# Kernel optimization log

Measured on AMD Instinct MI355X. Metric: run time of the kernel, lower is better.

The kernel has to match this reference:

```python
import jax, jax.numpy as jnp
import numpy as np

TIMESTEPS = 8
NUM_HEADS = 16
CTX = 1024
D = 1024
HD = D // NUM_HEADS
LN_EPS = 1e-5


def setup_inputs() -> dict:
    key = jax.random.key(0)
    ks = jax.random.split(key, 16)
    s = 0.02
    return {
        "current_embs": jax.random.normal(ks[0], (4, CTX, D), jnp.float32),
        "emb_table": jax.random.normal(ks[1], (TIMESTEPS, D), jnp.float32) * s,
        "Wq": jax.random.normal(ks[2], (NUM_HEADS, D, HD), jnp.float32) * s,
        "Wk": jax.random.normal(ks[3], (NUM_HEADS, D, HD), jnp.float32) * s,
        "Wv": jax.random.normal(ks[4], (NUM_HEADS, D, HD), jnp.float32) * s,
        "fc_w": jax.random.normal(ks[5], (D, D), jnp.float32) * s,
        "fc_b": jnp.zeros((D,), jnp.float32),
        "ln1_w": jnp.ones((D,), jnp.float32),
        "ln1_b": jnp.zeros((D,), jnp.float32),
        "ln2_w": jnp.ones((D,), jnp.float32),
        "ln2_b": jnp.zeros((D,), jnp.float32),
        "mlp_w1": jax.random.normal(ks[6], (D, 2 * D), jnp.float32) * s,
        "mlp_b1": jnp.zeros((2 * D,), jnp.float32),
        "mlp_w2": jax.random.normal(ks[7], (2 * D, D), jnp.float32) * s,
        "mlp_b2": jnp.zeros((D,), jnp.float32),
        "mlp_w3": jax.random.normal(ks[8], (D, D), jnp.float32) * s,
        "mlp_b3": jnp.zeros((D,), jnp.float32),
    }


def _layernorm(x, w, b):
    mu = jnp.mean(x, axis=-1, keepdims=True)
    var = jnp.var(x, axis=-1, keepdims=True)
    return (x - mu) * jax.lax.rsqrt(var + LN_EPS) * w + b


def _block(x, Wq, Wk, Wv, fc_w, fc_b, ln1_w, ln1_b, ln2_w, ln2_b,
           mlp_w1, mlp_b1, mlp_w2, mlp_b2, mlp_w3, mlp_b3):
    B, T, C = x.shape
    h = _layernorm(x, ln1_w, ln1_b)
    # per-head projections: [B,H,T,HD]
    q = jnp.einsum("btd,hdk->bhtk", h, Wq)
    k = jnp.einsum("btd,hdk->bhtk", h, Wk)
    v = jnp.einsum("btd,hdk->bhtk", h, Wv)
    # NOTE: original scales by embed_size**-0.5 (C), not head_dim**-0.5
    wei = jnp.einsum("bhtk,bhsk->bhts", q, k) * (C ** -0.5)
    causal = jnp.tril(jnp.ones((T, T), bool))
    wei = jnp.where(causal, wei, -jnp.inf)
    wei = jax.nn.softmax(wei, axis=-1)
    attn = jnp.einsum("bhts,bhsk->bhtk", wei, v)  # [B,H,T,HD]
    attn = attn.transpose(0, 2, 1, 3).reshape(B, T, C)  # concat heads
    sa = attn @ fc_w + fc_b
    x = x + sa  # dropout is identity in eval mode
    h2 = _layernorm(x, ln2_w, ln2_b)
    m = ((h2 @ mlp_w1 + mlp_b1) @ mlp_w2 + mlp_b2) @ mlp_w3 + mlp_b3
    m = jax.nn.gelu(m, approximate=False)  # GELU after three stacked Linears, as in source
    return x + m


def reference(current_embs, emb_table, Wq, Wk, Wv, fc_w, fc_b,
              ln1_w, ln1_b, ln2_w, ln2_b,
              mlp_w1, mlp_b1, mlp_w2, mlp_b2, mlp_w3, mlp_b3):
    new_embs = current_embs
    for i in range(TIMESTEPS):
        current_embs = current_embs + new_embs + emb_table[i][None, None, :]
        new_embs = _block(current_embs, Wq, Wk, Wv, fc_w, fc_b,
                          ln1_w, ln1_b, ln2_w, ln2_b,
                          mlp_w1, mlp_b1, mlp_w2, mlp_b2, mlp_w3, mlp_b3)
    return new_embs
```

## Files before the change

### kernel.cpp

```cpp
#include <hip/hip_runtime.h>
#include <hip/hip_bf16.h>
#include <math.h>

typedef __bf16 bf16;
typedef __bf16 bf16x8 __attribute__((ext_vector_type(8)));
typedef __bf16 bf16x4 __attribute__((ext_vector_type(4)));
typedef short  s16x4  __attribute__((ext_vector_type(4)));
typedef float  f32x4  __attribute__((ext_vector_type(4)));

#define MFMA32(a,b,c) __builtin_amdgcn_mfma_f32_16x16x32_bf16((a),(b),(c),0,0,0)
#define MFMA16(a,b,c) __builtin_amdgcn_mfma_f32_16x16x16bf16_1k((a),(b),(c),0,0,0)
#define EXP2F(x) __builtin_amdgcn_exp2f(x)
#define GLL16(gp, lp) __builtin_amdgcn_global_load_lds(\
    (const __attribute__((address_space(1))) void*)(gp), \
    (__attribute__((address_space(3))) void*)(lp), 16, 0, 0)

__device__ __forceinline__ float wave_sum(float v){
#pragma unroll
  for(int off=1; off<64; off<<=1) v += __shfl_xor(v, off);
  return v;
}

__global__ __launch_bounds__(256) void add_ln_kernel(
    const float* __restrict__ xsrc, const float* __restrict__ addsrc,
    const float* __restrict__ emb,
    const float* __restrict__ gw, const float* __restrict__ gb,
    float* __restrict__ xout, bf16* __restrict__ hout)
{
  const int row = blockIdx.x;
  const int t = threadIdx.x;
  const size_t rbase = (size_t)row * 1024;
  float4 x = ((const float4*)(xsrc + rbase))[t];
  if(addsrc){
    float4 a = ((const float4*)(addsrc + rbase))[t];
    x.x += a.x; x.y += a.y; x.z += a.z; x.w += a.w;
  }
  if(emb){
    float4 e = ((const float4*)emb)[t];
    x.x += e.x; x.y += e.y; x.z += e.z; x.w += e.w;
  }
  if(xout) ((float4*)(xout + rbase))[t] = x;

  float s = x.x + x.y + x.z + x.w;
  float q = x.x*x.x + x.y*x.y + x.z*x.z + x.w*x.w;
  s = wave_sum(s); q = wave_sum(q);
  __shared__ float red[8];
  const int w = t >> 6;
  if((t & 63) == 0){ red[w] = s; red[4+w] = q; }
  __syncthreads();
  s = red[0]+red[1]+red[2]+red[3];
  q = red[4]+red[5]+red[6]+red[7];
  const float mean = s * (1.0f/1024.0f);
  const float var  = q * (1.0f/1024.0f) - mean*mean;
  const float inv  = rsqrtf(var + 1e-5f);

  float4 wv = ((const float4*)gw)[t];
  float4 bv = ((const float4*)gb)[t];
  bf16x4 hv;
  hv[0] = (bf16)((x.x - mean)*inv*wv.x + bv.x);
  hv[1] = (bf16)((x.y - mean)*inv*wv.y + bv.y);
  hv[2] = (bf16)((x.z - mean)*inv*wv.z + bv.z);
  hv[3] = (bf16)((x.w - mean)*inv*wv.w + bv.w);
  *(bf16x4*)(hout + rbase + t*4) = hv;
}

__global__ __launch_bounds__(256) void pack_all_kernel(
    const float* __restrict__ Wq, const float* __restrict__ Wk, const float* __restrict__ Wv,
    const float* __restrict__ fcw, const float* __restrict__ w2,
    const float* __restrict__ w3,  const float* __restrict__ w1,
    bf16* __restrict__ wqkvT, bf16* __restrict__ fcT,
    bf16* __restrict__ w2T,   bf16* __restrict__ w3T, bf16* __restrict__ w1pl)
{
  const int bid = blockIdx.x;
  const int tid = threadIdx.x;
  if(bid >= 1792){
    const int i0 = (bid-1792)*2048 + tid*8;
    float4 a = *(const float4*)(w1 + i0);
    float4 b = *(const float4*)(w1 + i0 + 4);
    bf16x8 o;
    o[0]=(bf16)a.x; o[1]=(bf16)a.y; o[2]=(bf16)a.z; o[3]=(bf16)a.w;
    o[4]=(bf16)b.x; o[5]=(bf16)b.y; o[6]=(bf16)b.z; o[7]=(bf16)b.w;
    *(bf16x8*)(w1pl + i0) = o;
    return;
  }

  __shared__ float tile[64][65];
  const float* src; bf16* dst;
  int src_ld, dst_ld;
  if(bid < 768){
    const int seg = bid >> 8, r8 = bid & 255;
    const int h = r8 >> 4, d0 = (r8 & 15)*64;
    const float* W = (seg==0) ? Wq : (seg==1 ? Wk : Wv);
    src = W + h*65536 + (size_t)d0*64;  src_ld = 64;
    dst = wqkvT + ((size_t)(seg*1024 + h*64))*1024 + d0;  dst_ld = 1024;
  } else if(bid < 1024){
    const int t2 = bid - 768;
    const int k0 = (t2 >> 4)*64, n0 = (t2 & 15)*64;
    src = fcw + (size_t)k0*1024 + n0;  src_ld = 1024;
    dst = fcT + (size_t)n0*1024 + k0;  dst_ld = 1024;
  } else if(bid < 1536){
    const int t2 = bid - 1024;
    const int k0 = (t2 >> 4)*64, n0 = (t2 & 15)*64;
    src = w2 + (size_t)k0*1024 + n0;  src_ld = 1024;
    dst = w2T + (size_t)n0*2048 + k0;  dst_ld = 2048;
  } else {
    const int t2 = bid - 1536;
    const int k0 = (t2 >> 4)*64, n0 = (t2 & 15)*64;
    src = w3 + (size_t)k0*1024 + n0;  src_ld = 1024;
    dst = w3T + (size_t)n0*1024 + k0;  dst_ld = 1024;
  }

  {
    const int r = tid >> 4, c4 = (tid & 15)*4;
#pragma unroll
    for(int p=0; p<4; p++){
      float4 v = *(const float4*)(src + (size_t)(r + 16*p)*src_ld + c4);
      tile[r+16*p][c4]   = v.x;
      tile[r+16*p][c4+1] = v.y;
      tile[r+16*p][c4+2] = v.z;
      tile[r+16*p][c4+3] = v.w;
    }
  }
  __syncthreads();
  {
    const int n = tid >> 2, k16 = (tid & 3)*16;
#pragma unroll
    for(int half=0; half<2; half++){
      bf16x8 o;
#pragma unroll
      for(int j=0; j<8; j++) o[j] = (bf16)tile[k16 + half*8 + j][n];
      *(bf16x8*)(dst + (size_t)n*dst_ld + k16 + half*8) = o;
    }
  }
}

__global__ __launch_bounds__(256) void biasmv_kernel(const float* __restrict__ bin, const bf16* __restrict__ WT,
                                                     const float* __restrict__ badd, float* __restrict__ out, int Kd){
  const int n = blockIdx.x, t = threadIdx.x;
  float acc = 0.f;
  for(int k=t; k<Kd; k+=256) acc += bin[k]*(float)WT[(size_t)n*Kd + k];
  acc = wave_sum(acc);
  __shared__ float red[4];
  if((t&63)==0) red[t>>6] = acc;
  __syncthreads();
  if(t==0) out[n] = red[0]+red[1]+red[2]+red[3] + badd[n];
}

template<int EPI, int BLKM, int KH>
__global__ __launch_bounds__(256,2) void gemm_kernel(
    const bf16* __restrict__ A, const bf16* __restrict__ Bt,
    float* __restrict__ outf, bf16* __restrict__ outb,
    bf16* __restrict__ o2, bf16* __restrict__ o3,
    const float* __restrict__ bias, const float* __restrict__ res,
    const float* __restrict__ res2, const float* __restrict__ embn,
    int N, int K)
{
  constexpr int RM = BLKM/32;
  constexpr int HM = BLKM/2;
  constexpr int AISS = BLKM/32;
  __shared__ __align__(16) bf16 As[KH*BLKM*64];
  __shared__ __align__(16) bf16 Bs[KH*128*64];
  const int tid = threadIdx.x, w = tid>>6, lane = tid&63;
  const int quad = lane>>4, l16 = lane&15;
  const int wm = w&1, wn = w>>1;
  const int tn = blockIdx.x, tm = blockIdx.y;

  const int srow = lane>>3;
  const int sch  = (lane&7) ^ srow;
  const bf16* Ag = A  + (size_t)(tm*BLKM + w*8 + srow)*K + sch*8;
  const bf16* Bg = Bt + (size_t)(tn*128  + w*8 + srow)*K + sch*8;

  f32x4 acc[RM][4] = {};

  for(int k0 = 0; k0 < K; k0 += 64*KH){
#pragma unroll
    for(int h=0; h<KH; h++){
#pragma unroll
      for(int i=0;i<AISS;i++) GLL16(Ag + h*64 + (size_t)(i*32)*K, As + h*(BLKM*64) + (w*8 + i*32)*64);
#pragma unroll
      for(int i=0;i<4;i++)    GLL16(Bg + h*64 + (size_t)(i*32)*K, Bs + h*(128*64) + (w*8 + i*32)*64);
    }
    Ag += 64*KH; Bg += 64*KH;
    __syncthreads();
#pragma unroll
    for(int h=0; h<KH; h++){
      const bf16* Ash = As + h*(BLKM*64);
      const bf16* Bsh = Bs + h*(128*64);
      bf16x8 af[RM][2], bfr[4][2];
#pragma unroll
      for(int r=0;r<RM;r++){
        const int row = wm*HM + r*16 + l16;
        const bf16* rp = Ash + row*64;
#pragma unroll
        for(int kc=0;kc<2;kc++)
          af[r][kc] = *(const bf16x8*)(rp + ((kc*4+quad) ^ (row&7))*8);
      }
#pragma unroll
      for(int c=0;c<4;c++){
        const int row = wn*64 + c*16 + l16;
        const bf16* rp = Bsh + row*64;
#pragma unroll
        for(int kc=0;kc<2;kc++)
          bfr[c][kc] = *(const bf16x8*)(rp + ((kc*4+quad) ^ (row&7))*8);
      }
#pragma unroll
      for(int kc=0;kc<2;kc++)
#pragma unroll
        for(int r=0;r<RM;r++)
#pragma unroll
          for(int c=0;c<4;c++)
            acc[r][c] = MFMA32(af[r][kc], bfr[c][kc], acc[r][c]);
    }
    __syncthreads();
  }

#pragma unroll
  for(int r=0;r<RM;r++){
    const int grow0 = tm*BLKM + wm*HM + r*16 + quad*4;
#pragma unroll
    for(int c=0;c<4;c++){
      const int gcol = tn*128 + wn*64 + c*16 + l16;
      float bv = 0.0f;
      if constexpr (EPI>=1 && EPI!=4) bv = bias[gcol];
      if constexpr (EPI==4){
        const int seg = gcol >> 10;
        if(seg < 2){
          bf16* op = (seg==0) ? outb : o2;
          const float qs = (seg==0) ? 0.045084439f : 1.0f;
          const int col = gcol & 1023;
#pragma unroll
          for(int g=0; g<4; g++)
            op[(size_t)(grow0+g)*1024 + col] = (bf16)(acc[r][c][g]*qs);
        } else {
          const int col0 = gcol & 1023, hh = col0>>6, kk = col0&63;
          const int btok = grow0>>10, t0 = grow0&1023;
          bf16x4 pv;
#pragma unroll
          for(int g=0; g<4; g++) pv[g] = (bf16)acc[r][c][g];
          *(bf16x4*)(o3 + ((size_t)(btok*16+hh)*64 + kk)*1024 + t0) = pv;
        }
      } else {
        const float ev = (EPI==5) ? embn[gcol] : 0.0f;
#pragma unroll
        for(int g=0; g<4; g++){
          const float vv = acc[r][c][g] + bv;
          const size_t idx = (size_t)(grow0+g)*N + gcol;
          if constexpr (EPI<=1){
            outb[idx] = (bf16)vv;
          } else if constexpr (EPI==2){
            outf[idx] = res[idx] + vv;
          } else if constexpr (EPI==3){
            const float gel = 0.5f*vv*(1.0f + erff(vv*0.70710678118654752f));
            outf[idx] = res[idx] + gel;
          } else {
            const float gel = 0.5f*vv*(1.0f + erff(vv*0.70710678118654752f));
            outf[idx] = res[idx] + gel + res2[idx] + ev;
          }
        }
      }
    }
  }
}

constexpr int KSZ = 64*64;

__global__ __launch_bounds__(256,4) void attn_kernel(
    const bf16* __restrict__ Q, const bf16* __restrict__ Km,
    const bf16* __restrict__ Vt, bf16* __restrict__ O)
{
  __shared__ __align__(16) bf16 Ks[2*KSZ];
  __shared__ __align__(16) bf16 Vs[2*KSZ];
  const int qt = blockIdx.y;
  const int bh = blockIdx.x;
  const int b = bh >> 4, h = bh & 15;
  const int tid = threadIdx.x;
  const int w = tid>>6, lane = tid&63, quad = lane>>4, l16 = lane&15;
  const size_t qbase = (size_t)b*1024*1024 + (size_t)h*64;
  const size_t vbase = (size_t)(bh*64)*1024;
  const int qrow0 = qt*64 + w*16;
  const int myrow = qrow0 + l16;

  const bf16* qp = Q + qbase + (size_t)myrow*1024 + quad*8;
  bf16x8 bq0 = *(const bf16x8*)qp, bq1 = *(const bf16x8*)(qp + 32);

  f32x4 o[4] = {};
  float l = 0.f;
  const f32x4 zf = {0.f,0.f,0.f,0.f};

  const bf16* kg = Km + qbase + (size_t)(w*8 + (lane>>3))*1024 + ((lane&7)^(lane>>3))*8;
  const bf16* vg = Vt + vbase + (size_t)(w*8 + (lane>>3))*1024 + ((lane&7)^(lane>>3))*8;

  GLL16(kg,                       Ks + w*512);
  GLL16(kg + (size_t)32*1024,     Ks + 2048 + w*512);
  GLL16(vg,                       Vs + w*512);
  GLL16(vg + (size_t)32*1024,     Vs + 2048 + w*512);

  for(int kb = 0; kb <= qt; kb++){
    const int cur = kb & 1;
    __syncthreads();

    if(kb < qt){
      const bf16* kgp = kg + (size_t)(kb+1)*64*1024;
      const bf16* vgp = vg + (size_t)(kb+1)*64;
      bf16* kd = Ks + (cur^1)*KSZ + w*512;
      bf16* vd = Vs + (cur^1)*KSZ + w*512;
      GLL16(kgp,                   kd);
      GLL16(kgp + (size_t)32*1024, kd + 2048);
      GLL16(vgp,                   vd);
      GLL16(vgp + (size_t)32*1024, vd + 2048);
    }

    const bool diag = (kb == qt);
    const int nc = diag ? (w+1) : 4;
    const bf16* ksb = Ks + cur*KSZ;
    const bf16* vsb = Vs + cur*KSZ;

    f32x4 s[4];
#pragma unroll
    for(int c=0;c<4;c++){
      if(c >= nc) continue;
      const int row = c*16 + l16;
      const bf16* rp = ksb + row*64;
      bf16x8 ak0 = *(const bf16x8*)(rp + (( quad      ^ (row&7))<<3));
      bf16x8 ak1 = *(const bf16x8*)(rp + (((quad^4)   ^ (row&7))<<3));
      s[c] = MFMA32(ak0, bq0, zf);
      s[c] = MFMA32(ak1, bq1, s[c]);
    }

    s16x4 pp[4];
#pragma unroll
    for(int c=0;c<4;c++){
      if(c >= nc) continue;
      bf16x4 pb;
#pragma unroll
      for(int g=0;g<4;g++){
        const int key = kb*64 + c*16 + quad*4 + g;
        const float e = (diag && key > myrow) ? 0.f : EXP2F(s[c][g]);
        l += e; pb[g] = (bf16)e;
      }
      pp[c] = __builtin_bit_cast(s16x4, pb);
    }

#pragma unroll
    for(int c=0;c<4;c++){
      if(c >= nc) continue;
#pragma unroll
      for(int d=0;d<4;d++){
        const int row = d*16 + l16;
        const int eo  = ((((c*2 + (quad>>1)) ^ (row&7))<<3) + ((quad&1)<<2));
        bf16x4 av = *(const bf16x4*)(vsb + row*64 + eo);
        o[d] = MFMA16(__builtin_bit_cast(s16x4, av), pp[c], o[d]);
      }
    }
  }

  l += __shfl_xor(l, 16); l += __shfl_xor(l, 32);

  __syncthreads();
  {
    bf16* ot = Ks + w*(16*72);
    const float inv = 1.0f / l;
#pragma unroll
    for(int d=0;d<4;d++)
#pragma unroll
      for(int g=0;g<4;g++)
        ot[l16*72 + d*16 + quad*4 + g] = (bf16)(o[d][g]*inv);
#pragma unroll
    for(int p2=0;p2<2;p2++){
      const int qr = (lane>>3) + 8*p2, hd0 = (lane&7)*8;
      bf16x8 val = *(const bf16x8*)(ot + qr*72 + hd0);
      *(bf16x8*)(O + qbase + (size_t)(qrow0+qr)*1024 + hd0) = val;
    }
  }
}

extern "C" void kernel_launch(void* const* d_in, const int* in_sizes, int n_in,
                              void* d_out, int out_size, void* d_ws, size_t ws_size,
                              hipStream_t stream)
{
  const float* x_in = (const float*)d_in[0];
  const float* emb  = (const float*)d_in[1];
  const float* Wq   = (const float*)d_in[2];
  const float* Wk   = (const float*)d_in[3];
  const float* Wv   = (const float*)d_in[4];
  const float* fcw  = (const float*)d_in[5];
  const float* fcb  = (const float*)d_in[6];
  const float* ln1w = (const float*)d_in[7];
  const float* ln1b = (const float*)d_in[8];
  const float* ln2w = (const float*)d_in[9];
  const float* ln2b = (const float*)d_in[10];
  const float* w1   = (const float*)d_in[11];
  const float* b1   = (const float*)d_in[12];
  const float* w2   = (const float*)d_in[13];
  const float* b2   = (const float*)d_in[14];
  const float* w3   = (const float*)d_in[15];
  const float* b3   = (const float*)d_in[16];

  char* ws = (char*)d_ws;
  const size_t MB = 1024*1024;
  float* cur    = (float*)(ws + 0);
  float* x1     = (float*)(ws + 16*MB);
  bf16*  hb     = (bf16*)(ws + 48*MB);
  bf16*  attnb  = (bf16*)(ws + 56*MB);
  bf16*  qb     = (bf16*)(ws + 64*MB);
  bf16*  kbuf   = (bf16*)(ws + 72*MB);
  bf16*  vtb    = (bf16*)(ws + 80*MB);
  bf16*  w1pl   = (bf16*)(ws + 88*MB);
  bf16*  T12    = (bf16*)(ws + 92*MB);
  bf16*  wqkvT  = (bf16*)(ws + 96*MB);
  bf16*  fcT    = (bf16*)(ws + 102*MB);
  bf16*  w2T    = (bf16*)(ws + 104*MB);
  bf16*  w3T    = (bf16*)(ws + 108*MB);
  bf16*  WeffT  = (bf16*)(ws + 110*MB);
  float* tmpb   = (float*)(ws + 112*MB);
  float* beff   = (float*)(ws + 112*MB + 8192);

  pack_all_kernel<<<2816,256,0,stream>>>(Wq, Wk, Wv, fcw, w2, w3, w1,
                                         wqkvT, fcT, w2T, w3T, w1pl);
  gemm_kernel<0,64,2><<<dim3(8,16),256,0,stream>>>(w1pl, w2T, nullptr, T12,   nullptr, nullptr, nullptr, nullptr, nullptr, nullptr, 1024, 2048);
  gemm_kernel<0,64,2><<<dim3(8,16),256,0,stream>>>(w3T,  T12, nullptr, WeffT, nullptr, nullptr, nullptr, nullptr, nullptr, nullptr, 1024, 1024);
  biasmv_kernel<<<1024,256,0,stream>>>(b1,   w2T, b2, tmpb, 2048);
  biasmv_kernel<<<1024,256,0,stream>>>(tmpb, w3T, b3, beff, 1024);

  add_ln_kernel<<<4096,256,0,stream>>>(x_in, x_in, emb, ln1w, ln1b, cur, hb);
  for(int t=0; t<8; t++){
    if(t > 0)
      add_ln_kernel<<<4096,256,0,stream>>>(cur, nullptr, nullptr, ln1w, ln1b, nullptr, hb);
    gemm_kernel<4,128,1><<<dim3(24,32),256,0,stream>>>(hb, wqkvT, nullptr, qb, kbuf, vtb, nullptr, nullptr, nullptr, nullptr, 3072, 1024);
    attn_kernel<<<dim3(64,16),256,0,stream>>>(qb, kbuf, vtb, attnb);
    gemm_kernel<2,64,2><<<dim3(8,64),256,0,stream>>>(attnb, fcT, x1, nullptr, nullptr, nullptr, fcb, cur, nullptr, nullptr, 1024, 1024);
    add_ln_kernel<<<4096,256,0,stream>>>(x1, nullptr, nullptr, ln2w, ln2b, nullptr, hb);
    if(t < 7)
      gemm_kernel<5,64,2><<<dim3(8,64),256,0,stream>>>(hb, WeffT, cur, nullptr, nullptr, nullptr, beff, x1, cur, emb + (t+1)*1024, 1024, 1024);
    else
      gemm_kernel<3,64,2><<<dim3(8,64),256,0,stream>>>(hb, WeffT, (float*)d_out, nullptr, nullptr, nullptr, beff, x1, nullptr, nullptr, 1024, 1024);
  }
}
```

Measured before the change: 1.061 ms.

## Balance causal attention work by pairing query tiles and splitting long rows

The causal attention kernel previously gave each block one query tile, so block work ranged from 1 to 16 key tiles. Now each of 16 blocks per head processes exactly 9 key tiles: blocks 0-7 handle a short tile qA=s plus the first half of a long tile qB=15-s, while blocks 8-15 handle the remaining half of long tiles. Partial unnormalized outputs and row sums for the long tiles are written to fp32 scratch, and a new combine kernel sums them and normalizes. This adds an extra launch and fp32 partial traffic in exchange for removing the load imbalance of the causal tail.

```diff
diff --git a/kernel.cpp b/kernel.cpp
--- a/kernel.cpp
+++ b/kernel.cpp
@@ -266,42 +266,59 @@
 
 __global__ __launch_bounds__(256,4) void attn_kernel(
     const bf16* __restrict__ Q, const bf16* __restrict__ Km,
-    const bf16* __restrict__ Vt, bf16* __restrict__ O)
+    const bf16* __restrict__ Vt, bf16* __restrict__ O,
+    float* __restrict__ po, float* __restrict__ pl)
 {
-  __shared__ __align__(16) bf16 Ks[2*KSZ];
-  __shared__ __align__(16) bf16 Vs[2*KSZ];
-  const int qt = blockIdx.y;
+  __shared__ __align__(16) char smem[32768];
+  bf16* Ks = (bf16*)smem;
+  bf16* Vs = (bf16*)(smem + 16384);
+
+  const int s  = blockIdx.y;
   const int bh = blockIdx.x;
   const int b = bh >> 4, h = bh & 15;
   const int tid = threadIdx.x;
   const int w = tid>>6, lane = tid&63, quad = lane>>4, l16 = lane&15;
   const size_t qbase = (size_t)b*1024*1024 + (size_t)h*64;
   const size_t vbase = (size_t)(bh*64)*1024;
-  const int qrow0 = qt*64 + w*16;
-  const int myrow = qrow0 + l16;
-
-  const bf16* qp = Q + qbase + (size_t)myrow*1024 + quad*8;
-  bf16x8 bq0 = *(const bf16x8*)qp, bq1 = *(const bf16x8*)(qp + 32);
-
-  f32x4 o[4] = {};
-  float l = 0.f;
+
+  const bool two = (s < 8);
+  const int qA = s;
+  const int qB = two ? (15 - s) : s;
+  const int aN = two ? (s + 1) : 0;
+  const int bLo = two ? 0 : (s - 7);
+  const int total = aN + (two ? (8 - s) : 8);
+
+  const int rowA = qA*64 + w*16 + l16;
+  const int rowB = qB*64 + w*16 + l16;
+
+  const bf16* qpA = Q + qbase + (size_t)rowA*1024 + quad*8;
+  const bf16* qpB = Q + qbase + (size_t)rowB*1024 + quad*8;
+  bf16x8 bqA0 = *(const bf16x8*)qpA, bqA1 = *(const bf16x8*)(qpA + 32);
+  bf16x8 bqB0 = *(const bf16x8*)qpB, bqB1 = *(const bf16x8*)(qpB + 32);
+
+  f32x4 oA[4] = {}, oB[4] = {};
+  float lA = 0.f, lB = 0.f;
   const f32x4 zf = {0.f,0.f,0.f,0.f};
 
   const bf16* kg = Km + qbase + (size_t)(w*8 + (lane>>3))*1024 + ((lane&7)^(lane>>3))*8;
   const bf16* vg = Vt + vbase + (size_t)(w*8 + (lane>>3))*1024 + ((lane&7)^(lane>>3))*8;
 
-  GLL16(kg,                       Ks + w*512);
-  GLL16(kg + (size_t)32*1024,     Ks + 2048 + w*512);
-  GLL16(vg,                       Vs + w*512);
-  GLL16(vg + (size_t)32*1024,     Vs + 2048 + w*512);
-
-  for(int kb = 0; kb <= qt; kb++){
-    const int cur = kb & 1;
+  {
+    const int kb0 = two ? 0 : bLo;
+    GLL16(kg + (size_t)kb0*64*1024,                   Ks + w*512);
+    GLL16(kg + (size_t)kb0*64*1024 + (size_t)32*1024, Ks + 2048 + w*512);
+    GLL16(vg + kb0*64,                                Vs + w*512);
+    GLL16(vg + kb0*64 + (size_t)32*1024,              Vs + 2048 + w*512);
+  }
+
+  for(int u = 0; u < total; u++){
+    const int cur = u & 1;
     __syncthreads();
 
-    if(kb < qt){
-      const bf16* kgp = kg + (size_t)(kb+1)*64*1024;
-      const bf16* vgp = vg + (size_t)(kb+1)*64;
+    if(u + 1 < total){
+      const int kbn = (u+1 < aN) ? (u+1) : (bLo + (u+1) - aN);
+      const bf16* kgp = kg + (size_t)kbn*64*1024;
+      const bf16* vgp = vg + kbn*64;
       bf16* kd = Ks + (cur^1)*KSZ + w*512;
       bf16* vd = Vs + (cur^1)*KSZ + w*512;
       GLL16(kgp,                   kd);
@@ -310,12 +327,15 @@
       GLL16(vgp + (size_t)32*1024, vd + 2048);
     }
 
-    const bool diag = (kb == qt);
+    const bool inA = (u < aN);
+    const int kb = inA ? u : (bLo + u - aN);
+    const bool diag = inA ? (kb == qA) : (!two && (u == total-1));
     const int nc = diag ? (w+1) : 4;
+    const int myrow = inA ? rowA : rowB;
     const bf16* ksb = Ks + cur*KSZ;
     const bf16* vsb = Vs + cur*KSZ;
 
-    f32x4 s[4];
+    f32x4 sx[4];
 #pragma unroll
     for(int c=0;c<4;c++){
       if(c >= nc) continue;
@@ -323,11 +343,17 @@
       const bf16* rp = ksb + row*64;
       bf16x8 ak0 = *(const bf16x8*)(rp + (( quad      ^ (row&7))<<3));
       bf16x8 ak1 = *(const bf16x8*)(rp + (((quad^4)   ^ (row&7))<<3));
-      s[c] = MFMA32(ak0, bq0, zf);
-      s[c] = MFMA32(ak1, bq1, s[c]);
+      if(inA){
+        sx[c] = MFMA32(ak0, bqA0, zf);
+        sx[c] = MFMA32(ak1, bqA1, sx[c]);
+      } else {
+        sx[c] = MFMA32(ak0, bqB0, zf);
+        sx[c] = MFMA32(ak1, bqB1, sx[c]);
+      }
     }
 
     s16x4 pp[4];
+    float lacc = 0.f;
 #pragma unroll
     for(int c=0;c<4;c++){
       if(c >= nc) continue;
@@ -335,11 +361,12 @@
 #pragma unroll
       for(int g=0;g<4;g++){
         const int key = kb*64 + c*16 + quad*4 + g;
-        const float e = (diag && key > myrow) ? 0.f : EXP2F(s[c][g]);
-        l += e; pb[g] = (bf16)e;
+        const float e = (diag && key > myrow) ? 0.f : EXP2F(sx[c][g]);
+        lacc += e; pb[g] = (bf16)e;
       }
       pp[c] = __builtin_bit_cast(s16x4, pb);
     }
+    if(inA) lA += lacc; else lB += lacc;
 
 #pragma unroll
     for(int c=0;c<4;c++){
@@ -349,29 +376,82 @@
         const int row = d*16 + l16;
         const int eo  = ((((c*2 + (quad>>1)) ^ (row&7))<<3) + ((quad&1)<<2));
         bf16x4 av = *(const bf16x4*)(vsb + row*64 + eo);
-        o[d] = MFMA16(__builtin_bit_cast(s16x4, av), pp[c], o[d]);
+        if(inA) oA[d] = MFMA16(__builtin_bit_cast(s16x4, av), pp[c], oA[d]);
+        else    oB[d] = MFMA16(__builtin_bit_cast(s16x4, av), pp[c], oB[d]);
       }
     }
   }
 
-  l += __shfl_xor(l, 16); l += __shfl_xor(l, 32);
+  lA += __shfl_xor(lA, 16); lA += __shfl_xor(lA, 32);
+  lB += __shfl_xor(lB, 16); lB += __shfl_xor(lB, 32);
 
   __syncthreads();
-  {
-    bf16* ot = Ks + w*(16*72);
-    const float inv = 1.0f / l;
+
+  if(two){
+    bf16* ot = (bf16*)smem + w*(16*72);
+    const float inv = 1.0f / lA;
 #pragma unroll
     for(int d=0;d<4;d++)
 #pragma unroll
       for(int g=0;g<4;g++)
-        ot[l16*72 + d*16 + quad*4 + g] = (bf16)(o[d][g]*inv);
+        ot[l16*72 + d*16 + quad*4 + g] = (bf16)(oA[d][g]*inv);
 #pragma unroll
     for(int p2=0;p2<2;p2++){
       const int qr = (lane>>3) + 8*p2, hd0 = (lane&7)*8;
       bf16x8 val = *(const bf16x8*)(ot + qr*72 + hd0);
-      *(bf16x8*)(O + qbase + (size_t)(qrow0+qr)*1024 + hd0) = val;
-    }
-  }
+      *(bf16x8*)(O + qbase + (size_t)(qA*64 + w*16 + qr)*1024 + hd0) = val;
+    }
+  }
+
+  const int pslot = ((bh*8 + (qB-8))<<1) + (two ? 0 : 1);
+  if(quad == 0) pl[pslot*64 + w*16 + l16] = lB;
+  float* ot32 = (float*)(smem + 9216);
+#pragma unroll
+  for(int d=0;d<4;d++)
+#pragma unroll
+    for(int g=0;g<4;g++)
+      ot32[(w*16 + l16)*65 + d*16 + quad*4 + g] = oB[d][g];
+  __syncthreads();
+  {
+    const int r = tid>>2, c16 = (tid&3)*16;
+    float* dst = po + (size_t)pslot*4096 + r*64 + c16;
+#pragma unroll
+    for(int j=0;j<4;j++){
+      float4 v;
+      v.x = ot32[r*65 + c16 + 4*j];
+      v.y = ot32[r*65 + c16 + 4*j + 1];
+      v.z = ot32[r*65 + c16 + 4*j + 2];
+      v.w = ot32[r*65 + c16 + 4*j + 3];
+      *(float4*)(dst + 4*j) = v;
+    }
+  }
+}
+
+__global__ __launch_bounds__(256) void attn_combine_kernel(
+    const float* __restrict__ po, const float* __restrict__ pl, bf16* __restrict__ O)
+{
+  const int bh = blockIdx.x, qth = blockIdx.y;
+  const int b = bh >> 4, h = bh & 15;
+  const int qt = 8 + qth;
+  const int t = threadIdx.x;
+  const int r = t >> 2, c16 = (t & 3) * 16;
+  const size_t base0 = ((size_t)(bh*8 + qth)*2)*4096 + r*64 + c16;
+  const size_t base1 = base0 + 4096;
+  const float lsum = pl[(bh*8+qth)*128 + r] + pl[(bh*8+qth)*128 + 64 + r];
+  const float inv = 1.0f / lsum;
+  __align__(16) bf16 outv[16];
+#pragma unroll
+  for(int j=0;j<4;j++){
+    float4 a = *(const float4*)(po + base0 + 4*j);
+    float4 c = *(const float4*)(po + base1 + 4*j);
+    outv[4*j  ] = (bf16)((a.x + c.x)*inv);
+    outv[4*j+1] = (bf16)((a.y + c.y)*inv);
+    outv[4*j+2] = (bf16)((a.z + c.z)*inv);
+    outv[4*j+3] = (bf16)((a.w + c.w)*inv);
+  }
+  bf16* op = O + (size_t)b*1024*1024 + (size_t)(qt*64 + r)*1024 + h*64 + c16;
+  *(bf16x8*)op     = *(bf16x8*)outv;
+  *(bf16x8*)(op+8) = *(bf16x8*)(outv+8);
 }
 
 extern "C" void kernel_launch(void* const* d_in, const int* in_sizes, int n_in,
@@ -400,6 +480,7 @@
   const size_t MB = 1024*1024;
   float* cur    = (float*)(ws + 0);
   float* x1     = (float*)(ws + 16*MB);
+  float* po     = (float*)(ws + 32*MB);
   bf16*  hb     = (bf16*)(ws + 48*MB);
   bf16*  attnb  = (bf16*)(ws + 56*MB);
   bf16*  qb     = (bf16*)(ws + 64*MB);
@@ -414,6 +495,7 @@
   bf16*  WeffT  = (bf16*)(ws + 110*MB);
   float* tmpb   = (float*)(ws + 112*MB);
   float* beff   = (float*)(ws + 112*MB + 8192);
+  float* pl     = (float*)(ws + 114*MB);
 
   pack_all_kernel<<<2816,256,0,stream>>>(Wq, Wk, Wv, fcw, w2, w3, w1,
                                          wqkvT, fcT, w2T, w3T, w1pl);
@@ -427,7 +509,8 @@
     if(t > 0)
       add_ln_kernel<<<4096,256,0,stream>>>(cur, nullptr, nullptr, ln1w, ln1b, nullptr, hb);
     gemm_kernel<4,128,1><<<dim3(24,32),256,0,stream>>>(hb, wqkvT, nullptr, qb, kbuf, vtb, nullptr, nullptr, nullptr, nullptr, 3072, 1024);
-    attn_kernel<<<dim3(64,16),256,0,stream>>>(qb, kbuf, vtb, attnb);
+    attn_kernel<<<dim3(64,16),256,0,stream>>>(qb, kbuf, vtb, attnb, po, pl);
+    attn_combine_kernel<<<dim3(64,8),256,0,stream>>>(po, pl, attnb);
     gemm_kernel<2,64,2><<<dim3(8,64),256,0,stream>>>(attnb, fcT, x1, nullptr, nullptr, nullptr, fcb, cur, nullptr, nullptr, 1024, 1024);
     add_ln_kernel<<<4096,256,0,stream>>>(x1, nullptr, nullptr, ln2w, ln2b, nullptr, hb);
     if(t < 7)
```

New measurement: 1.097 ms. 3.4% more time.
